# Kernel optimization log

Hardware: AMD Instinct MI355X
Metric: run time of the kernel (lower is better)

## Reference

```python
import jax, jax.numpy as jnp
import numpy as np

B, T, H = 8, 8192, 512
E, R = 4, 16
SCALE = 0.04  # ~1/sqrt(H), keeps activations/logits in a sane range


def setup_inputs() -> dict:
    key = jax.random.key(0)
    ks = jax.random.split(key, 7)
    return {
        "x": jax.random.normal(ks[0], (B, T, H), jnp.float32),
        "gate_w": jax.random.normal(ks[1], (E, H), jnp.float32) * SCALE,
        "thr_w": jax.random.normal(ks[2], (1, H), jnp.float32) * SCALE,
        "fc1_w": jax.random.normal(ks[3], (E, H, H), jnp.float32) * SCALE,
        "lora_A": jax.random.normal(ks[4], (E, H, R), jnp.float32) * SCALE,
        "lora_B": jax.random.normal(ks[5], (E, R, H), jnp.float32) * SCALE,
        "fc2_w": jax.random.normal(ks[6], (E, H, H), jnp.float32) * SCALE,
    }


def reference(x, gate_w, thr_w, fc1_w, lora_A, lora_B, fc2_w):
    b, t, h = x.shape
    e = gate_w.shape[0]
    xf = x.reshape(-1, h)  # [N, H], N = B*T

    # Threshold-gated routing
    gate_logits = jax.nn.softmax(xf @ gate_w.T, axis=-1)          # [N, E]
    thresholds = jax.nn.sigmoid(xf @ thr_w.T) * (1.0 / e)         # [N, 1]
    adapted = gate_logits - thresholds                            # [N, E]
    selected = (adapted >= 0).astype(xf.dtype)                    # [N, E]
    weights = adapted * selected
    wsum = jnp.sum(weights, axis=-1, keepdims=True)
    wsum = jnp.where(wsum == 0, jnp.ones_like(wsum), wsum)
    weights = weights / wsum                                      # [N, E]

    # Experts: fc2(relu(fc1(x)) @ A @ B). Dense over all experts; the
    # weighted combine with zero weights matches the gather/scatter path.
    hidden = jax.nn.relu(jnp.einsum('ni,ehi->neh', xf, fc1_w))    # [N, E, H]
    lo = jnp.einsum('neh,ehr->ner', hidden, lora_A)               # [N, E, R]
    lo = jnp.einsum('ner,ero->neo', lo, lora_B)                   # [N, E, H]
    expert_out = jnp.einsum('neo,edo->ned', lo, fc2_w)            # [N, E, H]

    out = jnp.einsum('ne,ned->nd', weights, expert_out)           # [N, H]
    return out.reshape(b, t, h)
```

## Files before the change

### kernel.cpp

```cpp
#include <hip/hip_runtime.h>
#include <stdint.h>

#define NTOK 65536
#define HD   512
#define EXP  4
#define RK   16

typedef __attribute__((ext_vector_type(8)))  short short8;
typedef __attribute__((ext_vector_type(4)))  float f32x4;
typedef __attribute__((ext_vector_type(16))) float f32x16;

__device__ __forceinline__ unsigned short f2bf(float f) {
  union { float f; unsigned int u; } c; c.f = f;
  return (unsigned short)((c.u + 0x7fffu + ((c.u >> 16) & 1u)) >> 16);
}

__device__ __forceinline__ void gl_lds16(const void* g, void* l) {
  __builtin_amdgcn_global_load_lds((const __attribute__((address_space(1))) void*)g,
                                   (__attribute__((address_space(3))) void*)l, 16, 0, 0);
}

__global__ void convgate(const float* __restrict__ x, const float* __restrict__ gw,
                         const float* __restrict__ tw, unsigned short* __restrict__ xbo,
                         float* __restrict__ gates) {
  const int lane = threadIdx.x & 63;
  const int n = blockIdx.x * 4 + (threadIdx.x >> 6);
  const float4* xr = (const float4*)(x + (size_t)n * HD);
  const float4 xa = xr[lane * 2], xb = xr[lane * 2 + 1];
  ushort4 ua, ub;
  ua.x = f2bf(xa.x); ua.y = f2bf(xa.y); ua.z = f2bf(xa.z); ua.w = f2bf(xa.w);
  ub.x = f2bf(xb.x); ub.y = f2bf(xb.y); ub.z = f2bf(xb.z); ub.w = f2bf(xb.w);
  ushort4* xo = (ushort4*)(xbo + (size_t)n * HD);
  xo[lane * 2] = ua; xo[lane * 2 + 1] = ub;
  float s[5];
#pragma unroll
  for (int e = 0; e < 4; e++) {
    const float4* wr = (const float4*)(gw + e * HD);
    const float4 wa = wr[lane * 2], wb = wr[lane * 2 + 1];
    s[e] = xa.x * wa.x + xa.y * wa.y + xa.z * wa.z + xa.w * wa.w
         + xb.x * wb.x + xb.y * wb.y + xb.z * wb.z + xb.w * wb.w;
  }
  {
    const float4* wr = (const float4*)tw;
    const float4 wa = wr[lane * 2], wb = wr[lane * 2 + 1];
    s[4] = xa.x * wa.x + xa.y * wa.y + xa.z * wa.z + xa.w * wa.w
         + xb.x * wb.x + xb.y * wb.y + xb.z * wb.z + xb.w * wb.w;
  }
#pragma unroll
  for (int off = 32; off > 0; off >>= 1)
#pragma unroll
    for (int i = 0; i < 5; i++) s[i] += __shfl_xor(s[i], off, 64);
  float m = fmaxf(fmaxf(s[0], s[1]), fmaxf(s[2], s[3]));
  float e0 = expf(s[0] - m), e1 = expf(s[1] - m), e2 = expf(s[2] - m), e3 = expf(s[3] - m);
  float inv = 1.f / (e0 + e1 + e2 + e3);
  float thr = 0.25f / (1.f + expf(-s[4]));
  float a0 = e0 * inv - thr, a1 = e1 * inv - thr, a2 = e2 * inv - thr, a3 = e3 * inv - thr;
  float w0 = a0 > 0.f ? a0 : 0.f, w1 = a1 > 0.f ? a1 : 0.f;
  float w2 = a2 > 0.f ? a2 : 0.f, w3 = a3 > 0.f ? a3 : 0.f;
  float wsum = w0 + w1 + w2 + w3;
  wsum = (wsum == 0.f) ? 1.f : wsum;
  if (lane < 4) {
    float wv = lane == 0 ? w0 : lane == 1 ? w1 : lane == 2 ? w2 : w3;
    gates[(size_t)n * 4 + lane] = wv / wsum;
  }
}

__global__ void convk(const float* __restrict__ in, unsigned short* __restrict__ o, int n4) {
  int i = blockIdx.x * 256 + threadIdx.x;
  if (i < n4) {
    float4 v = ((const float4*)in)[i];
    ushort4 u;
    u.x = f2bf(v.x); u.y = f2bf(v.y); u.z = f2bf(v.z); u.w = f2bf(v.w);
    ((ushort4*)o)[i] = u;
  }
}

__global__ void prep_mt(const float* __restrict__ loraB, const float* __restrict__ fc2,
                        unsigned short* __restrict__ Mt) {
  int idx = blockIdx.x * 256 + threadIdx.x;
  int d  = idx & (HD - 1);
  int er = idx >> 9;
  int e = er >> 4, r = er & 15;
  const float4* B = (const float4*)(loraB + ((size_t)e * RK + r) * HD);
  const float4* F = (const float4*)(fc2 + ((size_t)e * HD + d) * HD);
  float a0 = 0.f, a1 = 0.f, a2 = 0.f, a3 = 0.f;
  for (int i = 0; i < HD / 4; i += 4) {
    float4 b0 = B[i],     f0 = F[i];
    float4 b1 = B[i + 1], f1 = F[i + 1];
    float4 b2 = B[i + 2], f2 = F[i + 2];
    float4 b3 = B[i + 3], f3 = F[i + 3];
    a0 += b0.x * f0.x + b0.y * f0.y + b0.z * f0.z + b0.w * f0.w;
    a1 += b1.x * f1.x + b1.y * f1.y + b1.z * f1.z + b1.w * f1.w;
    a2 += b2.x * f2.x + b2.y * f2.y + b2.z * f2.z + b2.w * f2.w;
    a3 += b3.x * f3.x + b3.y * f3.y + b3.z * f3.z + b3.w * f3.w;
  }
  Mt[d * 64 + er] = f2bf(a0 + a1 + a2 + a3);
}

__launch_bounds__(512, 2)
__global__ void fc1_lora(const unsigned short* __restrict__ xb,
                         const unsigned short* __restrict__ w1b,
                         const float* __restrict__ loraA,
                         float* __restrict__ lw) {
  __shared__ __align__(16) char smem[135168];
  const int bid = blockIdx.x;
  const int c = bid & 7;
  const int j = bid >> 3;
  const int eh = j & 7;
  const int e = eh >> 1, hq = eh & 1;
  const int ntile = c * 32 + (j >> 3);
  const int n0 = ntile * 256;
  const int tid = threadIdx.x;
  const int wave = tid >> 6, lane = tid & 63;
  const int l16 = lane & 15, quad = lane >> 4;
  const int l32 = lane & 31, half = lane >> 5;
  const int wr = wave >> 2, wc = wave & 3;

  const unsigned short* xg = xb + (size_t)n0 * HD;
  const unsigned short* wg = w1b + ((size_t)e * HD + (size_t)hq * 256) * HD;

  const unsigned short* xsrc[2];
  const unsigned short* wsrc[2];
#pragma unroll
  for (int i = 0; i < 2; i++) {
    const int sl = tid + 512 * i;
    const int sr = sl >> 3, g8 = (sl & 7) ^ (sr & 7);
    const int row = sr * 2 + (g8 >> 2), g = g8 & 3;
    xsrc[i] = xg + (size_t)row * HD + g * 8;
    wsrc[i] = wg + (size_t)row * HD + g * 8;
  }
  const int wbase = wave * 1024;

  int axo[2][4], bxo[2][2];
#pragma unroll
  for (int kk = 0; kk < 2; kk++) {
#pragma unroll
    for (int mb = 0; mb < 4; mb++) {
      const int rowa = wr * 128 + mb * 32 + l32;
      const int sr = rowa >> 1, g8 = (rowa & 1) * 4 + kk * 2 + half;
      axo[kk][mb] = (sr * 8 + (g8 ^ (sr & 7))) * 16;
    }
#pragma unroll
    for (int nb = 0; nb < 2; nb++) {
      const int rowb = wc * 64 + nb * 32 + l32;
      const int sr = rowb >> 1, g8 = (rowb & 1) * 4 + kk * 2 + half;
      bxo[kk][nb] = (sr * 8 + (g8 ^ (sr & 7))) * 16;
    }
  }

  f32x16 acc[4][2];
#pragma unroll
  for (int mb = 0; mb < 4; mb++)
#pragma unroll
    for (int nb = 0; nb < 2; nb++)
#pragma unroll
      for (int r = 0; r < 16; r++) acc[mb][nb][r] = 0.f;

#pragma unroll
  for (int tt = 0; tt < 3; tt++) {
    char* As = smem + tt * 32768;
#pragma unroll
    for (int i = 0; i < 2; i++) gl_lds16(xsrc[i] + tt * 32, As + wbase + 8192 * i);
#pragma unroll
    for (int i = 0; i < 2; i++) gl_lds16(wsrc[i] + tt * 32, As + 16384 + wbase + 8192 * i);
  }
  asm volatile("s_waitcnt vmcnt(8)\n\ts_barrier" ::: "memory");
  __builtin_amdgcn_sched_barrier(0);

#pragma unroll
  for (int t = 0; t < 16; t++) {
    char* Ab = smem + (t & 3) * 32768;
    char* Bb = Ab + 16384;
    char* As = smem + ((t + 3) & 3) * 32768;
    const int kos = (t + 3) * 32;
#pragma unroll
    for (int p = 0; p < 2; p++) {
      short8 af[4], bf[2];
#pragma unroll
      for (int mb = 0; mb < 4; mb++) af[mb] = *(const short8*)(Ab + axo[p][mb]);
#pragma unroll
      for (int nb = 0; nb < 2; nb++) bf[nb] = *(const short8*)(Bb + bxo[p][nb]);
      if (t < 13) {
        gl_lds16(xsrc[p] + kos, As + wbase + 8192 * p);
        gl_lds16(wsrc[p] + kos, As + 16384 + wbase + 8192 * p);
      }
      asm volatile("s_barrier" ::: "memory");
      __builtin_amdgcn_s_setprio(1);
#pragma unroll
      for (int mb = 0; mb < 4; mb++)
#pragma unroll
        for (int nb = 0; nb < 2; nb++)
          acc[mb][nb] = __builtin_amdgcn_mfma_f32_32x32x16_bf16(af[mb], bf[nb], acc[mb][nb], 0, 0, 0);
      __builtin_amdgcn_s_setprio(0);
    }
    if (t < 13) {
      asm volatile("s_waitcnt lgkmcnt(0)\n\ts_waitcnt vmcnt(8)\n\ts_barrier" ::: "memory");
    } else if (t == 13) {
      asm volatile("s_waitcnt lgkmcnt(0)\n\ts_waitcnt vmcnt(4)\n\ts_barrier" ::: "memory");
    } else if (t == 14) {
      asm volatile("s_waitcnt lgkmcnt(0)\n\ts_waitcnt vmcnt(0)\n\ts_barrier" ::: "memory");
    } else {
      asm volatile("s_waitcnt lgkmcnt(0)\n\ts_barrier" ::: "memory");
    }
    __builtin_amdgcn_sched_barrier(0);
  }

  unsigned short* hsm = (unsigned short*)smem;
#pragma unroll
  for (int mb = 0; mb < 4; mb++)
#pragma unroll
    for (int nb = 0; nb < 2; nb++) {
      const int colh = wc * 64 + nb * 32 + l32;
#pragma unroll
      for (int r = 0; r < 16; r++) {
        const int tok = wr * 128 + mb * 32 + 4 * half + (r & 3) + 8 * (r >> 2);
        float v = acc[mb][nb][r];
        v = v > 0.f ? v : 0.f;
        hsm[tok * 264 + colh] = f2bf(v);
      }
    }
  __syncthreads();

  const float* Ae = loraA + (size_t)e * HD * RK;
  const int hA0 = hq * 256;
  f32x4 lo[2];
#pragma unroll
  for (int mf = 0; mf < 2; mf++)
#pragma unroll
    for (int i = 0; i < 4; i++) lo[mf][i] = 0.f;
#pragma unroll
  for (int k2 = 0; k2 < 8; k2++) {
    short8 a2[2];
#pragma unroll
    for (int mf = 0; mf < 2; mf++) {
      const int tok = wave * 32 + mf * 16 + l16;
      a2[mf] = *(const short8*)(hsm + tok * 264 + k2 * 32 + quad * 8);
    }
    union { short8 v; unsigned short sv[8]; } b2;
#pragma unroll
    for (int j2 = 0; j2 < 8; j2++)
      b2.sv[j2] = f2bf(Ae[(size_t)(hA0 + k2 * 32 + quad * 8 + j2) * RK + l16]);
#pragma unroll
    for (int mf = 0; mf < 2; mf++)
      lo[mf] = __builtin_amdgcn_mfma_f32_16x16x32_bf16(a2[mf], b2.v, lo[mf], 0, 0, 0);
  }
#pragma unroll
  for (int mf = 0; mf < 2; mf++)
#pragma unroll
    for (int i = 0; i < 4; i++)
      atomicAdd(lw + (size_t)(n0 + wave * 32 + mf * 16 + quad * 4 + i) * 64 + e * 16 + l16, lo[mf][i]);
}

__launch_bounds__(256, 2)
__global__ void combine_k(const float* __restrict__ lw, const float* __restrict__ gates,
                          const unsigned short* __restrict__ Mt, float* __restrict__ out) {
  __shared__ __align__(16) char smem[65536];
  const int n0 = blockIdx.x * 64;
  const int tid = threadIdx.x;
  const int wave = tid >> 6, lane = tid & 63, quad = lane >> 4, l16 = lane & 15;
#pragma unroll
  for (int i = 0; i < 16; i++) {
    const int slot = tid + 256 * i;
    const int row = slot >> 3;
    const int g = (slot & 7) ^ (row & 7);
    *(uint4*)(smem + slot * 16) = *(const uint4*)(Mt + row * 64 + g * 8);
  }
  __syncthreads();
  f32x4 acc[4][8];
#pragma unroll
  for (int a = 0; a < 4; a++)
#pragma unroll
    for (int b = 0; b < 8; b++)
#pragma unroll
      for (int i = 0; i < 4; i++) acc[a][b][i] = 0.f;
#pragma unroll
  for (int ks = 0; ks < 2; ks++) {
    short8 af[4], bfr[8];
#pragma unroll
    for (int mf = 0; mf < 4; mf++) {
      const int n = n0 + mf * 16 + l16;
      const float* lr = lw + (size_t)n * 64 + ks * 32 + quad * 8;
      float4 u0 = *(const float4*)lr;
      float4 u1 = *(const float4*)(lr + 4);
      const float g = gates[(size_t)n * 4 + ((ks * 32 + quad * 8) >> 4)];
      union { short8 v; unsigned short s[8]; } a;
      a.s[0] = f2bf(u0.x * g); a.s[1] = f2bf(u0.y * g);
      a.s[2] = f2bf(u0.z * g); a.s[3] = f2bf(u0.w * g);
      a.s[4] = f2bf(u1.x * g); a.s[5] = f2bf(u1.y * g);
      a.s[6] = f2bf(u1.z * g); a.s[7] = f2bf(u1.w * g);
      af[mf] = a.v;
    }
#pragma unroll
    for (int nf = 0; nf < 8; nf++) {
      const int row = wave * 128 + nf * 16 + l16;
      const int slot = row * 8 + ((ks * 4 + quad) ^ (row & 7));
      bfr[nf] = *(const short8*)(smem + slot * 16);
    }
#pragma unroll
    for (int mf = 0; mf < 4; mf++)
#pragma unroll
      for (int nf = 0; nf < 8; nf++)
        acc[mf][nf] = __builtin_amdgcn_mfma_f32_16x16x32_bf16(af[mf], bfr[nf], acc[mf][nf], 0, 0, 0);
  }
#pragma unroll
  for (int mf = 0; mf < 4; mf++)
#pragma unroll
    for (int nf = 0; nf < 8; nf++) {
      const int d = wave * 128 + nf * 16 + l16;
#pragma unroll
      for (int i = 0; i < 4; i++)
        out[(size_t)(n0 + mf * 16 + quad * 4 + i) * HD + d] = acc[mf][nf][i];
    }
}

extern "C" void kernel_launch(void* const* d_in, const int* in_sizes, int n_in,
                              void* d_out, int out_size, void* d_ws, size_t ws_size,
                              hipStream_t stream) {
  const float* x      = (const float*)d_in[0];
  const float* gate_w = (const float*)d_in[1];
  const float* thr_w  = (const float*)d_in[2];
  const float* fc1_w  = (const float*)d_in[3];
  const float* lora_A = (const float*)d_in[4];
  const float* lora_B = (const float*)d_in[5];
  const float* fc2_w  = (const float*)d_in[6];
  float* out = (float*)d_out;
  char* ws = (char*)d_ws;

  unsigned short* xbp = (unsigned short*)(ws);
  unsigned short* w1b = (unsigned short*)(ws + 67108864);
  unsigned short* Mt  = (unsigned short*)(ws + 69206016);
  float*          gts = (float*)(ws + 69271552);
  float*          lwp = (float*)(ws + 70320128);

  hipMemsetAsync(lwp, 0, (size_t)NTOK * 64 * sizeof(float), stream);
  convgate<<<NTOK / 4, 256, 0, stream>>>(x, gate_w, thr_w, xbp, gts);
  convk<<<1024, 256, 0, stream>>>(fc1_w, w1b, EXP * HD * HD / 4);
  prep_mt<<<128, 256, 0, stream>>>(lora_B, fc2_w, Mt);
  fc1_lora<<<2048, 512, 0, stream>>>(xbp, w1b, lora_A, lwp);
  combine_k<<<NTOK / 64, 256, 0, stream>>>(lwp, gts, Mt, out);
}
```

Measured before the change: 440.7 us.

## Shrink fc1 tile to 256x128 with 3-stage pipeline and pretransposed bf16 LoRA-A

The fc1+LoRA kernel now uses 256-thread blocks that each compute a 256-token by 128-hidden tile, replacing 512-thread blocks with 256-wide tiles. The grid doubles to 4096 blocks and LDS use falls from about 132KB to 72KB. The pipeline goes from four stages to three, with one barrier per k-step instead of several. A new prep kernel pre-converts and transposes lora_A to bf16, so the LoRA-A MFMA reads one vector per lane instead of eight strided fp32 loads with conversions. The trade-off is twice as many atomicAdds into the lw buffer and more reloading of the x tile across hidden quarters.

```diff
diff --git a/kernel.cpp b/kernel.cpp
--- a/kernel.cpp
+++ b/kernel.cpp
@@ -97,54 +97,67 @@
   Mt[d * 64 + er] = f2bf(a0 + a1 + a2 + a3);
 }
 
-__launch_bounds__(512, 2)
+__global__ void prep_la(const float* __restrict__ la, unsigned short* __restrict__ laT) {
+  int idx = blockIdx.x * 256 + threadIdx.x;
+  int h = idx & (HD - 1);
+  int er = idx >> 9;
+  int e = er >> 4, r = er & 15;
+  laT[(size_t)er * HD + h] = f2bf(la[((size_t)e * HD + h) * RK + r]);
+}
+
+__launch_bounds__(256, 2)
 __global__ void fc1_lora(const unsigned short* __restrict__ xb,
                          const unsigned short* __restrict__ w1b,
-                         const float* __restrict__ loraA,
+                         const unsigned short* __restrict__ laT,
                          float* __restrict__ lw) {
-  __shared__ __align__(16) char smem[135168];
+  __shared__ __align__(16) char smem[73728];
   const int bid = blockIdx.x;
   const int c = bid & 7;
   const int j = bid >> 3;
-  const int eh = j & 7;
-  const int e = eh >> 1, hq = eh & 1;
-  const int ntile = c * 32 + (j >> 3);
+  const int eh = j & 15;
+  const int e = eh >> 2, hq = eh & 3;
+  const int ntile = c * 32 + (j >> 4);
   const int n0 = ntile * 256;
   const int tid = threadIdx.x;
   const int wave = tid >> 6, lane = tid & 63;
   const int l16 = lane & 15, quad = lane >> 4;
   const int l32 = lane & 31, half = lane >> 5;
-  const int wr = wave >> 2, wc = wave & 3;
+  const int wr = wave >> 1, wc = wave & 1;
 
   const unsigned short* xg = xb + (size_t)n0 * HD;
-  const unsigned short* wg = w1b + ((size_t)e * HD + (size_t)hq * 256) * HD;
-
-  const unsigned short* xsrc[2];
+  const unsigned short* wg = w1b + ((size_t)e * HD + (size_t)hq * 128) * HD;
+
+  const unsigned short* xsrc[4];
   const unsigned short* wsrc[2];
 #pragma unroll
-  for (int i = 0; i < 2; i++) {
-    const int sl = tid + 512 * i;
+  for (int i = 0; i < 4; i++) {
+    const int sl = tid + 256 * i;
     const int sr = sl >> 3, g8 = (sl & 7) ^ (sr & 7);
     const int row = sr * 2 + (g8 >> 2), g = g8 & 3;
     xsrc[i] = xg + (size_t)row * HD + g * 8;
+  }
+#pragma unroll
+  for (int i = 0; i < 2; i++) {
+    const int sl = tid + 256 * i;
+    const int sr = sl >> 3, g8 = (sl & 7) ^ (sr & 7);
+    const int row = sr * 2 + (g8 >> 2), g = g8 & 3;
     wsrc[i] = wg + (size_t)row * HD + g * 8;
   }
-  const int wbase = wave * 1024;
 
   int axo[2][4], bxo[2][2];
 #pragma unroll
-  for (int kk = 0; kk < 2; kk++) {
+  for (int p = 0; p < 2; p++) {
 #pragma unroll
     for (int mb = 0; mb < 4; mb++) {
       const int rowa = wr * 128 + mb * 32 + l32;
-      const int sr = rowa >> 1, g8 = (rowa & 1) * 4 + kk * 2 + half;
-      axo[kk][mb] = (sr * 8 + (g8 ^ (sr & 7))) * 16;
+      const int sr = rowa >> 1, g8 = (rowa & 1) * 4 + p * 2 + half;
+      axo[p][mb] = (sr * 8 + (g8 ^ (sr & 7))) * 16;
     }
 #pragma unroll
     for (int nb = 0; nb < 2; nb++) {
       const int rowb = wc * 64 + nb * 32 + l32;
-      const int sr = rowb >> 1, g8 = (rowb & 1) * 4 + kk * 2 + half;
-      bxo[kk][nb] = (sr * 8 + (g8 ^ (sr & 7))) * 16;
+      const int sr = rowb >> 1, g8 = (rowb & 1) * 4 + p * 2 + half;
+      bxo[p][nb] = (sr * 8 + (g8 ^ (sr & 7))) * 16;
     }
   }
 
@@ -157,22 +170,28 @@
       for (int r = 0; r < 16; r++) acc[mb][nb][r] = 0.f;
 
 #pragma unroll
-  for (int tt = 0; tt < 3; tt++) {
-    char* As = smem + tt * 32768;
-#pragma unroll
-    for (int i = 0; i < 2; i++) gl_lds16(xsrc[i] + tt * 32, As + wbase + 8192 * i);
-#pragma unroll
-    for (int i = 0; i < 2; i++) gl_lds16(wsrc[i] + tt * 32, As + 16384 + wbase + 8192 * i);
-  }
-  asm volatile("s_waitcnt vmcnt(8)\n\ts_barrier" ::: "memory");
+  for (int tt = 0; tt < 2; tt++) {
+    char* As = smem + tt * 24576;
+#pragma unroll
+    for (int i = 0; i < 4; i++) gl_lds16(xsrc[i] + tt * 32, As + (256 * i + wave * 64) * 16);
+#pragma unroll
+    for (int i = 0; i < 2; i++) gl_lds16(wsrc[i] + tt * 32, As + 16384 + (256 * i + wave * 64) * 16);
+  }
+  asm volatile("s_waitcnt vmcnt(6)\n\ts_barrier" ::: "memory");
   __builtin_amdgcn_sched_barrier(0);
 
 #pragma unroll
   for (int t = 0; t < 16; t++) {
-    char* Ab = smem + (t & 3) * 32768;
+    char* Ab = smem + (t % 3) * 24576;
     char* Bb = Ab + 16384;
-    char* As = smem + ((t + 3) & 3) * 32768;
-    const int kos = (t + 3) * 32;
+    if (t < 14) {
+      char* As = smem + ((t + 2) % 3) * 24576;
+      const int kos = (t + 2) * 32;
+#pragma unroll
+      for (int i = 0; i < 4; i++) gl_lds16(xsrc[i] + kos, As + (256 * i + wave * 64) * 16);
+#pragma unroll
+      for (int i = 0; i < 2; i++) gl_lds16(wsrc[i] + kos, As + 16384 + (256 * i + wave * 64) * 16);
+    }
 #pragma unroll
     for (int p = 0; p < 2; p++) {
       short8 af[4], bf[2];
@@ -180,11 +199,6 @@
       for (int mb = 0; mb < 4; mb++) af[mb] = *(const short8*)(Ab + axo[p][mb]);
 #pragma unroll
       for (int nb = 0; nb < 2; nb++) bf[nb] = *(const short8*)(Bb + bxo[p][nb]);
-      if (t < 13) {
-        gl_lds16(xsrc[p] + kos, As + wbase + 8192 * p);
-        gl_lds16(wsrc[p] + kos, As + 16384 + wbase + 8192 * p);
-      }
-      asm volatile("s_barrier" ::: "memory");
       __builtin_amdgcn_s_setprio(1);
 #pragma unroll
       for (int mb = 0; mb < 4; mb++)
@@ -193,10 +207,8 @@
           acc[mb][nb] = __builtin_amdgcn_mfma_f32_32x32x16_bf16(af[mb], bf[nb], acc[mb][nb], 0, 0, 0);
       __builtin_amdgcn_s_setprio(0);
     }
-    if (t < 13) {
-      asm volatile("s_waitcnt lgkmcnt(0)\n\ts_waitcnt vmcnt(8)\n\ts_barrier" ::: "memory");
-    } else if (t == 13) {
-      asm volatile("s_waitcnt lgkmcnt(0)\n\ts_waitcnt vmcnt(4)\n\ts_barrier" ::: "memory");
+    if (t < 14) {
+      asm volatile("s_waitcnt lgkmcnt(0)\n\ts_waitcnt vmcnt(6)\n\ts_barrier" ::: "memory");
     } else if (t == 14) {
       asm volatile("s_waitcnt lgkmcnt(0)\n\ts_waitcnt vmcnt(0)\n\ts_barrier" ::: "memory");
     } else {
@@ -216,39 +228,32 @@
         const int tok = wr * 128 + mb * 32 + 4 * half + (r & 3) + 8 * (r >> 2);
         float v = acc[mb][nb][r];
         v = v > 0.f ? v : 0.f;
-        hsm[tok * 264 + colh] = f2bf(v);
+        hsm[tok * 136 + colh] = f2bf(v);
       }
     }
   __syncthreads();
 
-  const float* Ae = loraA + (size_t)e * HD * RK;
-  const int hA0 = hq * 256;
-  f32x4 lo[2];
-#pragma unroll
-  for (int mf = 0; mf < 2; mf++)
+  const unsigned short* laTe = laT + (size_t)(e * 16 + l16) * HD + hq * 128;
+  f32x4 lo[4];
+#pragma unroll
+  for (int mf = 0; mf < 4; mf++)
 #pragma unroll
     for (int i = 0; i < 4; i++) lo[mf][i] = 0.f;
 #pragma unroll
-  for (int k2 = 0; k2 < 8; k2++) {
-    short8 a2[2];
-#pragma unroll
-    for (int mf = 0; mf < 2; mf++) {
-      const int tok = wave * 32 + mf * 16 + l16;
-      a2[mf] = *(const short8*)(hsm + tok * 264 + k2 * 32 + quad * 8);
-    }
-    union { short8 v; unsigned short sv[8]; } b2;
-#pragma unroll
-    for (int j2 = 0; j2 < 8; j2++)
-      b2.sv[j2] = f2bf(Ae[(size_t)(hA0 + k2 * 32 + quad * 8 + j2) * RK + l16]);
-#pragma unroll
-    for (int mf = 0; mf < 2; mf++)
-      lo[mf] = __builtin_amdgcn_mfma_f32_16x16x32_bf16(a2[mf], b2.v, lo[mf], 0, 0, 0);
-  }
-#pragma unroll
-  for (int mf = 0; mf < 2; mf++)
+  for (int k2 = 0; k2 < 4; k2++) {
+    const short8 b2 = *(const short8*)(laTe + k2 * 32 + quad * 8);
+#pragma unroll
+    for (int mf = 0; mf < 4; mf++) {
+      const int tok = wave * 64 + mf * 16 + l16;
+      const short8 a2 = *(const short8*)(hsm + tok * 136 + k2 * 32 + quad * 8);
+      lo[mf] = __builtin_amdgcn_mfma_f32_16x16x32_bf16(a2, b2, lo[mf], 0, 0, 0);
+    }
+  }
+#pragma unroll
+  for (int mf = 0; mf < 4; mf++)
 #pragma unroll
     for (int i = 0; i < 4; i++)
-      atomicAdd(lw + (size_t)(n0 + wave * 32 + mf * 16 + quad * 4 + i) * 64 + e * 16 + l16, lo[mf][i]);
+      atomicAdd(lw + (size_t)(n0 + wave * 64 + mf * 16 + quad * 4 + i) * 64 + e * 16 + l16, lo[mf][i]);
 }
 
 __launch_bounds__(256, 2)
@@ -331,11 +336,13 @@
   unsigned short* Mt  = (unsigned short*)(ws + 69206016);
   float*          gts = (float*)(ws + 69271552);
   float*          lwp = (float*)(ws + 70320128);
+  unsigned short* laT = (unsigned short*)(ws + 87097344);
 
   hipMemsetAsync(lwp, 0, (size_t)NTOK * 64 * sizeof(float), stream);
   convgate<<<NTOK / 4, 256, 0, stream>>>(x, gate_w, thr_w, xbp, gts);
   convk<<<1024, 256, 0, stream>>>(fc1_w, w1b, EXP * HD * HD / 4);
   prep_mt<<<128, 256, 0, stream>>>(lora_B, fc2_w, Mt);
-  fc1_lora<<<2048, 512, 0, stream>>>(xbp, w1b, lora_A, lwp);
+  prep_la<<<128, 256, 0, stream>>>(lora_A, laT);
+  fc1_lora<<<4096, 256, 0, stream>>>(xbp, w1b, laT, lwp);
   combine_k<<<NTOK / 64, 256, 0, stream>>>(lwp, gts, Mt, out);
 }
```

New measurement: 444.4 us. No clear change (+0.8%).
